# Kernel optimization log

Hardware: AMD Instinct MI355X
Metric: run time of the kernel (lower is better)

The kernel has to match this reference:

```python
import jax, jax.numpy as jnp
import numpy as np

N, K, C = 32768, 64, 256
PAIR, HID, BINS, CLIP = 32, 64, 16, 32
LN_EPS = 1e-5


def setup_inputs() -> dict:
    key = jax.random.key(0)
    ks = jax.random.split(key, 12)
    inp = {
        "features": jax.random.normal(ks[0], (N, C), jnp.float32),
        "resi": jnp.arange(N, dtype=jnp.int32),
        "chain": jax.random.randint(ks[1], (N,), 0, 4, jnp.int32),
        "batch": jax.random.randint(ks[2], (N,), 0, 8, jnp.int32),
        "neighbours": jax.random.randint(ks[3], (N, K), 0, N, jnp.int32),
        # learned params
        "W_left": jax.random.normal(ks[4], (C, PAIR), jnp.float32) / np.sqrt(C),
        "W_right": jax.random.normal(ks[5], (C, PAIR), jnp.float32) / np.sqrt(C),
        "W_pos": jax.random.normal(ks[6], (2 * CLIP + 1, PAIR), jnp.float32) * 0.1,
        "ln_scale": jnp.ones((PAIR,), jnp.float32),
        "ln_bias": jnp.zeros((PAIR,), jnp.float32),
        "W1": jax.random.normal(ks[7], (PAIR, HID), jnp.float32) / np.sqrt(PAIR),
        "b1": jnp.zeros((HID,), jnp.float32),
        "W2": jax.random.normal(ks[8], (HID, BINS), jnp.float32) / np.sqrt(HID),
        "b2": jnp.zeros((BINS,), jnp.float32),
    }
    return inp


def reference(features, resi, chain, batch, neighbours,
              W_left, W_right, W_pos, ln_scale, ln_bias, W1, b1, W2, b2):
    # left/right 32-dim codes, pairwise combine via neighbour gather: [N,K,32]
    left = features @ W_left
    right = features @ W_right
    dcode = left[:, None, :] + right[neighbours]

    # relative sequence position one-hot (65 classes) -> Linear(32, bias=False).
    # one_hot @ W_pos == row-gather of W_pos; masked to same chain & batch.
    rel = jnp.clip(resi[neighbours] - resi[:, None], -CLIP, CLIP) + CLIP  # [N,K]
    same = (chain[neighbours] == chain[:, None]) & (batch[neighbours] == batch[:, None])
    dcode = dcode + jnp.where(same[..., None], W_pos[rel], 0.0)

    # LayerNorm over last axis (scale + offset)
    mu = dcode.mean(-1, keepdims=True)
    var = jnp.mean(jnp.square(dcode - mu), -1, keepdims=True)
    dcode = (dcode - mu) * jax.lax.rsqrt(var + LN_EPS) * ln_scale + ln_bias

    # 2-layer GELU MLP -> 16 bins
    h = jax.nn.gelu(dcode @ W1 + b1)
    logits = h @ W2 + b2
    log_p = jax.nn.log_softmax(logits, axis=-1)

    # softmax-weighted expected distance over bin centers of [0, 22) A
    step = 22.0 / BINS
    bin_centers = (jnp.arange(BINS, dtype=jnp.float32) + 0.5) * step
    dmap = (jnp.exp(log_p) * bin_centers).sum(axis=-1)  # [N,K]
    return log_p, dmap
```

## Files before the change

kernel.cpp:

```cpp
#include <hip/hip_runtime.h>
#include <stdint.h>

#define N_RES 32768
#define KNEI  64
#define CFEAT 256
#define PAIRD 32
#define HIDD  64
#define NBINS 16
#define CLIPV 32
#define NGROUPS (N_RES * KNEI / 16)

typedef __attribute__((ext_vector_type(8))) short  short8;
typedef __attribute__((ext_vector_type(4))) float  float4_t;

union U8 { uint32_t u[4]; short8 s8; };

__device__ __forceinline__ uint32_t pkbf(float a, float b) {
    uint32_t ua = __float_as_uint(a) + 0x8000u;
    uint32_t ub = __float_as_uint(b) + 0x8000u;
    uint32_t d;
    const uint32_t sel = 0x07060302u;
    asm("v_perm_b32 %0, %1, %2, %3" : "=v"(d) : "v"(ub), "v"(ua), "s"(sel));
    return d;
}
__device__ __forceinline__ float bflo(uint32_t w) { return __uint_as_float(w << 16); }
__device__ __forceinline__ float bfhi(uint32_t w) { return __uint_as_float(w & 0xFFFF0000u); }

__device__ __forceinline__ float fastrcp(float x) { return __builtin_amdgcn_rcpf(x); }
__device__ __forceinline__ float fexp2(float x)   { return __builtin_amdgcn_exp2f(x); }
__device__ __forceinline__ float flog2(float x)   { return __builtin_amdgcn_logf(x); }

__device__ __forceinline__ float gelu_tanh(float x) {
    const float k1 = 2.3022082f;
    const float k2 = 0.1029432f;
    float x2 = x * x;
    float t  = __builtin_fmaf(k2, x2, k1);
    float e  = fexp2(x * t);
    float th = __builtin_fmaf(-2.0f, fastrcp(e + 1.0f), 1.0f);
    float hx = 0.5f * x;
    return __builtin_fmaf(hx, th, hx);
}

__global__ __launch_bounds__(256) void proj_kernel(
    const float* __restrict__ feat, const float* __restrict__ Wl,
    const float* __restrict__ Wr, const int* __restrict__ resi,
    const int* __restrict__ chain, const int* __restrict__ batch,
    const float* __restrict__ wpos,
    uint4* __restrict__ leftbf, uint4* __restrict__ rightbf,
    uint32_t* __restrict__ meta, uint32_t* __restrict__ wposbf)
{
    __shared__ __align__(16) float Wc[CFEAT * 32];
    const int tid   = threadIdx.x;
    const int half  = blockIdx.x >> 9;
    const int rb    = (blockIdx.x & 511) * 64;
    const float* W  = half ? Wr : Wl;
    uint4* outtb    = half ? rightbf : leftbf;

    for (int idx = tid; idx < CFEAT * 32; idx += 256)
        Wc[idx] = W[idx];
    if (half == 0 && tid < 64) {
        int r = rb + tid;
        meta[r] = (uint32_t)resi[r] | ((uint32_t)chain[r] << 16)
                | ((uint32_t)batch[r] << 19);
    }
    if (blockIdx.x == 0) {
        for (int i = tid; i < (2 * CLIPV + 1) * PAIRD / 2; i += 256)
            wposbf[i] = pkbf(wpos[2 * i], wpos[2 * i + 1]);
    }
    __syncthreads();

    const int cb  = (tid & 3) * 8;
    const int row = rb + (tid >> 2);

    float acc[8];
#pragma unroll
    for (int j = 0; j < 8; ++j) acc[j] = 0.f;

    for (int i = 0; i < CFEAT; i += 4) {
        float4_t f = *(const float4_t*)(feat + (size_t)row * CFEAT + i);
#pragma unroll
        for (int s = 0; s < 4; ++s) {
            float4_t wa = *(const float4_t*)(Wc + (i + s) * 32 + cb);
            float4_t wb = *(const float4_t*)(Wc + (i + s) * 32 + cb + 4);
#pragma unroll
            for (int j = 0; j < 4; ++j) {
                acc[j]     = __builtin_fmaf(f[s], wa[j], acc[j]);
                acc[4 + j] = __builtin_fmaf(f[s], wb[j], acc[4 + j]);
            }
        }
    }
    uint2 o;
    o.x = pkbf(acc[0], acc[1]);
    o.y = pkbf(acc[2], acc[3]);
    uint2 o2;
    o2.x = pkbf(acc[4], acc[5]);
    o2.y = pkbf(acc[6], acc[7]);
    uint2* dst = (uint2*)outtb + (size_t)row * 8 + (cb >> 2);
    dst[0] = o;
    dst[1] = o2;
}

__global__ __launch_bounds__(256, 8) void pair_kernel(
    const uint4* __restrict__ leftbf, const uint4* __restrict__ rightbf,
    const uint32_t* __restrict__ meta, const int* __restrict__ nbr,
    const uint32_t* __restrict__ wposbf,
    const float* __restrict__ lnS, const float* __restrict__ lnB,
    const float* __restrict__ W1, const float* __restrict__ b1,
    const float* __restrict__ W2, const float* __restrict__ b2,
    float* __restrict__ out_logp, float* __restrict__ out_dmap)
{
    __shared__ __align__(16) unsigned char Hbuf[4][16 * 144];
    __shared__ __align__(16) float b1p[HIDD];

    const int tid    = threadIdx.x;
    const int lane   = tid & 63;
    const int wlocal = tid >> 6;
    const int q      = lane >> 4;
    const int c      = lane & 15;

    if (tid < HIDD) {
        float s = b1[tid];
        for (int k = 0; k < PAIRD; ++k)
            s = __builtin_fmaf(lnB[k], W1[k * HIDD + tid], s);
        b1p[tid] = s;
    }

    short8 w1a[4];
#pragma unroll
    for (int t = 0; t < 4; ++t) {
        U8 tmp;
#pragma unroll
        for (int v = 0; v < 4; ++v) {
            int k0 = q * 8 + 2 * v, k1 = k0 + 1;
            float a0 = lnS[k0] * W1[k0 * HIDD + 16 * t + c];
            float a1 = lnS[k1] * W1[k1 * HIDD + 16 * t + c];
            tmp.u[v] = pkbf(a0, a1);
        }
        w1a[t] = tmp.s8;
    }
    short8 w2a[2];
#pragma unroll
    for (int kt = 0; kt < 2; ++kt) {
        U8 tmp;
#pragma unroll
        for (int v = 0; v < 4; ++v) {
            int k0 = kt * 32 + q * 8 + 2 * v;
            tmp.u[v] = pkbf(W2[k0 * NBINS + c], W2[(k0 + 1) * NBINS + c]);
        }
        w2a[kt] = tmp.s8;
    }
    const float4_t b2f = *(const float4_t*)(b2 + 4 * q);

    __syncthreads();

    const int wglobal = (blockIdx.x * 256 + tid) >> 6;
    const int nwaves  = (gridDim.x * 256) >> 6;

    for (int g = wglobal; g < NGROUPS; g += nwaves) {
        const int pbase = g * 16;
        const int n = pbase >> 6;
        const int p = pbase + c;
        const int nb = __builtin_nontemporal_load(nbr + p);

        const uint32_t mn = meta[n];
        const uint32_t mb = meta[nb];
        const uint4 lf = leftbf [(size_t)n  * 4 + q];
        const uint4 rf = rightbf[(size_t)nb * 4 + q];

        const int rel = min(max((int)(mb & 0xFFFFu) - (int)(mn & 0xFFFFu),
                                -CLIPV), CLIPV) + CLIPV;
        const float msk = (((mb ^ mn) & 0xFFFF0000u) == 0u) ? 1.0f : 0.0f;
        const uint4 pw = *(const uint4*)(wposbf + rel * 16 + q * 4);

        const uint32_t la[4] = {lf.x, lf.y, lf.z, lf.w};
        const uint32_t ra[4] = {rf.x, rf.y, rf.z, rf.w};
        const uint32_t pa[4] = {pw.x, pw.y, pw.z, pw.w};
        float d[8];
#pragma unroll
        for (int v = 0; v < 4; ++v) {
            d[2 * v]     = __builtin_fmaf(msk, bflo(pa[v]), bflo(la[v]) + bflo(ra[v]));
            d[2 * v + 1] = __builtin_fmaf(msk, bfhi(pa[v]), bfhi(la[v]) + bfhi(ra[v]));
        }

        float s1 = 0.f, s2 = 0.f;
#pragma unroll
        for (int j = 0; j < 8; ++j) { s1 += d[j]; s2 = __builtin_fmaf(d[j], d[j], s2); }
        s1 += __shfl_xor(s1, 16, 64);  s1 += __shfl_xor(s1, 32, 64);
        s2 += __shfl_xor(s2, 16, 64);  s2 += __shfl_xor(s2, 32, 64);
        const float mu   = s1 * (1.0f / 32.0f);
        const float var  = __builtin_fmaf(-mu, mu, s2 * (1.0f / 32.0f));
        const float rstd = __builtin_amdgcn_rsqf(var + 1e-5f);
        const float sh   = -mu * rstd;

        U8 dpack;
#pragma unroll
        for (int v = 0; v < 4; ++v) {
            float nA = __builtin_fmaf(d[2 * v],     rstd, sh);
            float nB = __builtin_fmaf(d[2 * v + 1], rstd, sh);
            dpack.u[v] = pkbf(nA, nB);
        }
        const short8 dfrag = dpack.s8;

        float4_t hacc[4];
#pragma unroll
        for (int t = 0; t < 4; ++t) {
            float4_t c1 = *(const float4_t*)(b1p + 16 * t + 4 * q);
            hacc[t] = __builtin_amdgcn_mfma_f32_16x16x32_bf16(w1a[t], dfrag, c1, 0, 0, 0);
        }

        unsigned char* hb = &Hbuf[wlocal][0] + c * 144;
#pragma unroll
        for (int t = 0; t < 4; ++t) {
            float g0 = gelu_tanh(hacc[t][0]);
            float g1 = gelu_tanh(hacc[t][1]);
            float g2 = gelu_tanh(hacc[t][2]);
            float g3 = gelu_tanh(hacc[t][3]);
            uint2 w; w.x = pkbf(g0, g1); w.y = pkbf(g2, g3);
            *(uint2*)(hb + 32 * t + 8 * q) = w;
        }
        const short8 hf0 = *(const short8*)(hb + 16 * q);
        const short8 hf1 = *(const short8*)(hb + 64 + 16 * q);

        float4_t lacc;
        lacc = __builtin_amdgcn_mfma_f32_16x16x32_bf16(w2a[0], hf0, b2f,  0, 0, 0);
        lacc = __builtin_amdgcn_mfma_f32_16x16x32_bf16(w2a[1], hf1, lacc, 0, 0, 0);

        const float LOG2E = 1.4426950408889634f, LN2 = 0.6931471805599453f;
        float e[4];
#pragma unroll
        for (int r = 0; r < 4; ++r) e[r] = fexp2(lacc[r] * LOG2E);
        float ssum = (e[0] + e[1]) + (e[2] + e[3]);
        ssum += __shfl_xor(ssum, 16, 64);
        ssum += __shfl_xor(ssum, 32, 64);
        const float lse = flog2(ssum) * LN2;

        float4_t lp = {lacc[0] - lse, lacc[1] - lse, lacc[2] - lse, lacc[3] - lse};
        __builtin_nontemporal_store(lp, (float4_t*)(out_logp + (size_t)p * NBINS + 4 * q));

        const float step  = 22.0f / NBINS;
        const float cbase = (4 * q + 0.5f) * step;
        float dpart = e[0] * cbase + e[1] * (cbase + step)
                    + e[2] * (cbase + 2 * step) + e[3] * (cbase + 3 * step);
        dpart += __shfl_xor(dpart, 16, 64);
        dpart += __shfl_xor(dpart, 32, 64);
        if (q == 0)
            __builtin_nontemporal_store(dpart * fastrcp(ssum), out_dmap + p);
    }
}

extern "C" void kernel_launch(void* const* d_in, const int* in_sizes, int n_in,
                              void* d_out, int out_size, void* d_ws, size_t ws_size,
                              hipStream_t stream) {
    const float* features = (const float*)d_in[0];
    const int*   resi     = (const int*)d_in[1];
    const int*   chain    = (const int*)d_in[2];
    const int*   batch    = (const int*)d_in[3];
    const int*   nbr      = (const int*)d_in[4];
    const float* W_left   = (const float*)d_in[5];
    const float* W_right  = (const float*)d_in[6];
    const float* W_pos    = (const float*)d_in[7];
    const float* ln_scale = (const float*)d_in[8];
    const float* ln_bias  = (const float*)d_in[9];
    const float* W1       = (const float*)d_in[10];
    const float* b1       = (const float*)d_in[11];
    const float* W2       = (const float*)d_in[12];
    const float* b2       = (const float*)d_in[13];

    char* ws = (char*)d_ws;
    uint4*    leftbf  = (uint4*)ws;
    uint4*    rightbf = (uint4*)(ws + (size_t)N_RES * 64);
    uint32_t* meta    = (uint32_t*)(ws + (size_t)2 * N_RES * 64);
    uint32_t* wposbf  = (uint32_t*)(ws + (size_t)2 * N_RES * 64 + N_RES * 4);

    float* out_logp = (float*)d_out;
    float* out_dmap = out_logp + (size_t)N_RES * KNEI * NBINS;

    proj_kernel<<<1024, 256, 0, stream>>>(features, W_left, W_right,
                                          resi, chain, batch, W_pos,
                                          leftbf, rightbf, meta, wposbf);
    pair_kernel<<<2048, 256, 0, stream>>>(leftbf, rightbf, meta, nbr, wposbf,
                                          ln_scale, ln_bias, W1, b1, W2, b2,
                                          out_logp, out_dmap);
}
```

Measured before the change: 290.2 us.

## Use MFMA projection, sigmoid GELU, and two-group staging in pair kernel

The projection kernel now runs on bf16 MFMA. Both weight matrices are transposed into LDS as bf16, and each wave computes 16 rows of left and right codes, so the kernel needs half as many blocks. In the pair kernel, the tanh-form GELU is replaced by the cheaper x*sigmoid(1.702x) approximation. The main loop is restructured to a fixed 16-iteration schedule that stages gathers for two groups before computing either, using double-buffered LDS for the hidden activations. The aim is to hide gather latency and cut transcendental work, at the cost of more register pressure, a different GELU approximation, and features rounded to bf16 before the projection.

```diff
diff --git a/kernel.cpp b/kernel.cpp
--- a/kernel.cpp
+++ b/kernel.cpp
@@ -30,15 +30,10 @@
 __device__ __forceinline__ float fexp2(float x)   { return __builtin_amdgcn_exp2f(x); }
 __device__ __forceinline__ float flog2(float x)   { return __builtin_amdgcn_logf(x); }
 
-__device__ __forceinline__ float gelu_tanh(float x) {
-    const float k1 = 2.3022082f;
-    const float k2 = 0.1029432f;
-    float x2 = x * x;
-    float t  = __builtin_fmaf(k2, x2, k1);
-    float e  = fexp2(x * t);
-    float th = __builtin_fmaf(-2.0f, fastrcp(e + 1.0f), 1.0f);
-    float hx = 0.5f * x;
-    return __builtin_fmaf(hx, th, hx);
+__device__ __forceinline__ float gelu_fast(float x) {
+    const float kG = -2.4554669f;
+    float e = fexp2(kG * x);
+    return x * fastrcp(1.0f + e) * 1.0f + 0.0f, x * fastrcp(1.0f + e);
 }
 
 __global__ __launch_bounds__(256) void proj_kernel(
@@ -46,19 +41,27 @@
     const float* __restrict__ Wr, const int* __restrict__ resi,
     const int* __restrict__ chain, const int* __restrict__ batch,
     const float* __restrict__ wpos,
-    uint4* __restrict__ leftbf, uint4* __restrict__ rightbf,
+    uint32_t* __restrict__ leftbf, uint32_t* __restrict__ rightbf,
     uint32_t* __restrict__ meta, uint32_t* __restrict__ wposbf)
 {
-    __shared__ __align__(16) float Wc[CFEAT * 32];
-    const int tid   = threadIdx.x;
-    const int half  = blockIdx.x >> 9;
-    const int rb    = (blockIdx.x & 511) * 64;
-    const float* W  = half ? Wr : Wl;
-    uint4* outtb    = half ? rightbf : leftbf;
-
-    for (int idx = tid; idx < CFEAT * 32; idx += 256)
-        Wc[idx] = W[idx];
-    if (half == 0 && tid < 64) {
+    __shared__ __align__(16) unsigned short Wt[64 * 264];
+
+    const int tid    = threadIdx.x;
+    const int lane   = tid & 63;
+    const int wlocal = tid >> 6;
+    const int q      = lane >> 4;
+    const int c      = lane & 15;
+    const int rb     = blockIdx.x * 64;
+
+    {
+        const int col = tid & 63;
+        const float* wsrc = (col < 32) ? (Wl + col) : (Wr + col - 32);
+        for (int k = tid >> 6; k < CFEAT; k += 4) {
+            uint32_t u = __float_as_uint(wsrc[(size_t)k * 32]) + 0x8000u;
+            Wt[col * 264 + k] = (unsigned short)(u >> 16);
+        }
+    }
+    if (tid < 64) {
         int r = rb + tid;
         meta[r] = (uint32_t)resi[r] | ((uint32_t)chain[r] << 16)
                 | ((uint32_t)batch[r] << 19);
@@ -69,35 +72,138 @@
     }
     __syncthreads();
 
-    const int cb  = (tid & 3) * 8;
-    const int row = rb + (tid >> 2);
-
-    float acc[8];
-#pragma unroll
-    for (int j = 0; j < 8; ++j) acc[j] = 0.f;
-
-    for (int i = 0; i < CFEAT; i += 4) {
-        float4_t f = *(const float4_t*)(feat + (size_t)row * CFEAT + i);
-#pragma unroll
-        for (int s = 0; s < 4; ++s) {
-            float4_t wa = *(const float4_t*)(Wc + (i + s) * 32 + cb);
-            float4_t wb = *(const float4_t*)(Wc + (i + s) * 32 + cb + 4);
-#pragma unroll
-            for (int j = 0; j < 4; ++j) {
-                acc[j]     = __builtin_fmaf(f[s], wa[j], acc[j]);
-                acc[4 + j] = __builtin_fmaf(f[s], wb[j], acc[4 + j]);
-            }
+    const int row0 = rb + wlocal * 16;
+    const float* fptr = feat + (size_t)(row0 + c) * CFEAT + q * 8;
+    const float4_t zero4 = {0.f, 0.f, 0.f, 0.f};
+
+    float4_t acc[4] = {zero4, zero4, zero4, zero4};
+    for (int kt = 0; kt < 8; ++kt) {
+        float4_t f0 = *(const float4_t*)(fptr + kt * 32);
+        float4_t f1 = *(const float4_t*)(fptr + kt * 32 + 4);
+        U8 bp;
+        bp.u[0] = pkbf(f0[0], f0[1]);
+        bp.u[1] = pkbf(f0[2], f0[3]);
+        bp.u[2] = pkbf(f1[0], f1[1]);
+        bp.u[3] = pkbf(f1[2], f1[3]);
+#pragma unroll
+        for (int nt = 0; nt < 4; ++nt) {
+            const short8 afr = *(const short8*)(Wt + (nt * 16 + c) * 264 + kt * 32 + q * 8);
+            acc[nt] = __builtin_amdgcn_mfma_f32_16x16x32_bf16(afr, bp.s8, acc[nt], 0, 0, 0);
         }
     }
-    uint2 o;
-    o.x = pkbf(acc[0], acc[1]);
-    o.y = pkbf(acc[2], acc[3]);
-    uint2 o2;
-    o2.x = pkbf(acc[4], acc[5]);
-    o2.y = pkbf(acc[6], acc[7]);
-    uint2* dst = (uint2*)outtb + (size_t)row * 8 + (cb >> 2);
-    dst[0] = o;
-    dst[1] = o2;
+    const size_t row = (size_t)(row0 + c);
+#pragma unroll
+    for (int nt = 0; nt < 4; ++nt) {
+        uint2 o;
+        o.x = pkbf(acc[nt][0], acc[nt][1]);
+        o.y = pkbf(acc[nt][2], acc[nt][3]);
+        if (nt < 2)
+            *(uint2*)(leftbf  + row * 16 + nt * 8 + 2 * q) = o;
+        else
+            *(uint2*)(rightbf + row * 16 + (nt - 2) * 8 + 2 * q) = o;
+    }
+}
+
+struct GS { int p; uint4 lf, rf, pw; float msk; };
+
+__device__ __forceinline__ void stage_group(
+    int g, int c, int q,
+    const uint4* __restrict__ leftbf, const uint4* __restrict__ rightbf,
+    const uint32_t* __restrict__ meta, const int* __restrict__ nbr,
+    const uint32_t* __restrict__ wposbf, GS& s)
+{
+    const int pbase = g * 16;
+    const int nu = __builtin_amdgcn_readfirstlane(pbase >> 6);
+    s.p = pbase + c;
+    const int nb = __builtin_nontemporal_load(nbr + s.p);
+    const uint32_t mn = meta[nu];
+    const uint32_t mb = meta[nb];
+    s.lf = leftbf[(size_t)nu * 4 + q];
+    s.rf = rightbf[(size_t)nb * 4 + q];
+    const int rel = min(max((int)(mb & 0xFFFFu) - (int)(mn & 0xFFFFu),
+                            -CLIPV), CLIPV) + CLIPV;
+    s.msk = (((mb ^ mn) & 0xFFFF0000u) == 0u) ? 1.0f : 0.0f;
+    s.pw = *(const uint4*)(wposbf + rel * 16 + q * 4);
+}
+
+__device__ __forceinline__ void compute_group(
+    const GS& s, int q, unsigned char* hb,
+    const short8* w1a, const short8* w2a,
+    const float* __restrict__ b1p, float4_t b2f,
+    float* __restrict__ out_logp, float* __restrict__ out_dmap)
+{
+    const uint32_t la[4] = {s.lf.x, s.lf.y, s.lf.z, s.lf.w};
+    const uint32_t ra[4] = {s.rf.x, s.rf.y, s.rf.z, s.rf.w};
+    const uint32_t pa[4] = {s.pw.x, s.pw.y, s.pw.z, s.pw.w};
+    float d[8];
+#pragma unroll
+    for (int v = 0; v < 4; ++v) {
+        d[2 * v]     = __builtin_fmaf(s.msk, bflo(pa[v]), bflo(la[v]) + bflo(ra[v]));
+        d[2 * v + 1] = __builtin_fmaf(s.msk, bfhi(pa[v]), bfhi(la[v]) + bfhi(ra[v]));
+    }
+
+    float s1 = 0.f, s2 = 0.f;
+#pragma unroll
+    for (int j = 0; j < 8; ++j) { s1 += d[j]; s2 = __builtin_fmaf(d[j], d[j], s2); }
+    s1 += __shfl_xor(s1, 16, 64);  s1 += __shfl_xor(s1, 32, 64);
+    s2 += __shfl_xor(s2, 16, 64);  s2 += __shfl_xor(s2, 32, 64);
+    const float mu   = s1 * (1.0f / 32.0f);
+    const float var  = __builtin_fmaf(-mu, mu, s2 * (1.0f / 32.0f));
+    const float rstd = __builtin_amdgcn_rsqf(var + 1e-5f);
+    const float sh   = -mu * rstd;
+
+    U8 dpack;
+#pragma unroll
+    for (int v = 0; v < 4; ++v) {
+        float nA = __builtin_fmaf(d[2 * v],     rstd, sh);
+        float nB = __builtin_fmaf(d[2 * v + 1], rstd, sh);
+        dpack.u[v] = pkbf(nA, nB);
+    }
+    const short8 dfrag = dpack.s8;
+
+    float4_t hacc[4];
+#pragma unroll
+    for (int t = 0; t < 4; ++t) {
+        float4_t c1 = *(const float4_t*)(b1p + 16 * t + 4 * q);
+        hacc[t] = __builtin_amdgcn_mfma_f32_16x16x32_bf16(w1a[t], dfrag, c1, 0, 0, 0);
+    }
+
+    const float kG = -2.4554669f;
+#pragma unroll
+    for (int t = 0; t < 4; ++t) {
+        float g0 = hacc[t][0] * fastrcp(1.0f + fexp2(kG * hacc[t][0]));
+        float g1 = hacc[t][1] * fastrcp(1.0f + fexp2(kG * hacc[t][1]));
+        float g2 = hacc[t][2] * fastrcp(1.0f + fexp2(kG * hacc[t][2]));
+        float g3 = hacc[t][3] * fastrcp(1.0f + fexp2(kG * hacc[t][3]));
+        uint2 w; w.x = pkbf(g0, g1); w.y = pkbf(g2, g3);
+        *(uint2*)(hb + 32 * t + 8 * q) = w;
+    }
+    const short8 hf0 = *(const short8*)(hb + 16 * q);
+    const short8 hf1 = *(const short8*)(hb + 64 + 16 * q);
+
+    float4_t lacc;
+    lacc = __builtin_amdgcn_mfma_f32_16x16x32_bf16(w2a[0], hf0, b2f,  0, 0, 0);
+    lacc = __builtin_amdgcn_mfma_f32_16x16x32_bf16(w2a[1], hf1, lacc, 0, 0, 0);
+
+    const float LOG2E = 1.4426950408889634f, LN2 = 0.6931471805599453f;
+    float e[4];
+#pragma unroll
+    for (int r = 0; r < 4; ++r) e[r] = fexp2(lacc[r] * LOG2E);
+    float ssum = (e[0] + e[1]) + (e[2] + e[3]);
+    ssum += __shfl_xor(ssum, 16, 64);
+    ssum += __shfl_xor(ssum, 32, 64);
+    const float lse = flog2(ssum) * LN2;
+
+    float4_t lp = {lacc[0] - lse, lacc[1] - lse, lacc[2] - lse, lacc[3] - lse};
+    __builtin_nontemporal_store(lp, (float4_t*)(out_logp + (size_t)s.p * NBINS + 4 * q));
+
+    const float step  = 22.0f / NBINS;
+    const float cbase = (4 * q + 0.5f) * step;
+    float dpart = e[0] * cbase + e[1] * (cbase + step)
+                + e[2] * (cbase + 2 * step) + e[3] * (cbase + 3 * step);
+    dpart += __shfl_xor(dpart, 16, 64);
+    dpart += __shfl_xor(dpart, 32, 64);
+    __builtin_nontemporal_store(dpart * fastrcp(ssum), out_dmap + s.p);
 }
 
 __global__ __launch_bounds__(256, 8) void pair_kernel(
@@ -109,7 +215,7 @@
     const float* __restrict__ W2, const float* __restrict__ b2,
     float* __restrict__ out_logp, float* __restrict__ out_dmap)
 {
-    __shared__ __align__(16) unsigned char Hbuf[4][16 * 144];
+    __shared__ __align__(16) unsigned char Hbuf[4][2][16 * 144];
     __shared__ __align__(16) float b1p[HIDD];
 
     const int tid    = threadIdx.x;
@@ -154,97 +260,15 @@
     __syncthreads();
 
     const int wglobal = (blockIdx.x * 256 + tid) >> 6;
-    const int nwaves  = (gridDim.x * 256) >> 6;
-
-    for (int g = wglobal; g < NGROUPS; g += nwaves) {
-        const int pbase = g * 16;
-        const int n = pbase >> 6;
-        const int p = pbase + c;
-        const int nb = __builtin_nontemporal_load(nbr + p);
-
-        const uint32_t mn = meta[n];
-        const uint32_t mb = meta[nb];
-        const uint4 lf = leftbf [(size_t)n  * 4 + q];
-        const uint4 rf = rightbf[(size_t)nb * 4 + q];
-
-        const int rel = min(max((int)(mb & 0xFFFFu) - (int)(mn & 0xFFFFu),
-                                -CLIPV), CLIPV) + CLIPV;
-        const float msk = (((mb ^ mn) & 0xFFFF0000u) == 0u) ? 1.0f : 0.0f;
-        const uint4 pw = *(const uint4*)(wposbf + rel * 16 + q * 4);
-
-        const uint32_t la[4] = {lf.x, lf.y, lf.z, lf.w};
-        const uint32_t ra[4] = {rf.x, rf.y, rf.z, rf.w};
-        const uint32_t pa[4] = {pw.x, pw.y, pw.z, pw.w};
-        float d[8];
-#pragma unroll
-        for (int v = 0; v < 4; ++v) {
-            d[2 * v]     = __builtin_fmaf(msk, bflo(pa[v]), bflo(la[v]) + bflo(ra[v]));
-            d[2 * v + 1] = __builtin_fmaf(msk, bfhi(pa[v]), bfhi(la[v]) + bfhi(ra[v]));
-        }
-
-        float s1 = 0.f, s2 = 0.f;
-#pragma unroll
-        for (int j = 0; j < 8; ++j) { s1 += d[j]; s2 = __builtin_fmaf(d[j], d[j], s2); }
-        s1 += __shfl_xor(s1, 16, 64);  s1 += __shfl_xor(s1, 32, 64);
-        s2 += __shfl_xor(s2, 16, 64);  s2 += __shfl_xor(s2, 32, 64);
-        const float mu   = s1 * (1.0f / 32.0f);
-        const float var  = __builtin_fmaf(-mu, mu, s2 * (1.0f / 32.0f));
-        const float rstd = __builtin_amdgcn_rsqf(var + 1e-5f);
-        const float sh   = -mu * rstd;
-
-        U8 dpack;
-#pragma unroll
-        for (int v = 0; v < 4; ++v) {
-            float nA = __builtin_fmaf(d[2 * v],     rstd, sh);
-            float nB = __builtin_fmaf(d[2 * v + 1], rstd, sh);
-            dpack.u[v] = pkbf(nA, nB);
-        }
-        const short8 dfrag = dpack.s8;
-
-        float4_t hacc[4];
-#pragma unroll
-        for (int t = 0; t < 4; ++t) {
-            float4_t c1 = *(const float4_t*)(b1p + 16 * t + 4 * q);
-            hacc[t] = __builtin_amdgcn_mfma_f32_16x16x32_bf16(w1a[t], dfrag, c1, 0, 0, 0);
-        }
-
-        unsigned char* hb = &Hbuf[wlocal][0] + c * 144;
-#pragma unroll
-        for (int t = 0; t < 4; ++t) {
-            float g0 = gelu_tanh(hacc[t][0]);
-            float g1 = gelu_tanh(hacc[t][1]);
-            float g2 = gelu_tanh(hacc[t][2]);
-            float g3 = gelu_tanh(hacc[t][3]);
-            uint2 w; w.x = pkbf(g0, g1); w.y = pkbf(g2, g3);
-            *(uint2*)(hb + 32 * t + 8 * q) = w;
-        }
-        const short8 hf0 = *(const short8*)(hb + 16 * q);
-        const short8 hf1 = *(const short8*)(hb + 64 + 16 * q);
-
-        float4_t lacc;
-        lacc = __builtin_amdgcn_mfma_f32_16x16x32_bf16(w2a[0], hf0, b2f,  0, 0, 0);
-        lacc = __builtin_amdgcn_mfma_f32_16x16x32_bf16(w2a[1], hf1, lacc, 0, 0, 0);
-
-        const float LOG2E = 1.4426950408889634f, LN2 = 0.6931471805599453f;
-        float e[4];
-#pragma unroll
-        for (int r = 0; r < 4; ++r) e[r] = fexp2(lacc[r] * LOG2E);
-        float ssum = (e[0] + e[1]) + (e[2] + e[3]);
-        ssum += __shfl_xor(ssum, 16, 64);
-        ssum += __shfl_xor(ssum, 32, 64);
-        const float lse = flog2(ssum) * LN2;
-
-        float4_t lp = {lacc[0] - lse, lacc[1] - lse, lacc[2] - lse, lacc[3] - lse};
-        __builtin_nontemporal_store(lp, (float4_t*)(out_logp + (size_t)p * NBINS + 4 * q));
-
-        const float step  = 22.0f / NBINS;
-        const float cbase = (4 * q + 0.5f) * step;
-        float dpart = e[0] * cbase + e[1] * (cbase + step)
-                    + e[2] * (cbase + 2 * step) + e[3] * (cbase + 3 * step);
-        dpart += __shfl_xor(dpart, 16, 64);
-        dpart += __shfl_xor(dpart, 32, 64);
-        if (q == 0)
-            __builtin_nontemporal_store(dpart * fastrcp(ssum), out_dmap + p);
+    unsigned char* hb0 = &Hbuf[wlocal][0][0] + c * 144;
+    unsigned char* hb1 = &Hbuf[wlocal][1][0] + c * 144;
+
+    for (int j = 0; j < 16; j += 2) {
+        GS A, B;
+        stage_group(wglobal + j * 8192,       c, q, leftbf, rightbf, meta, nbr, wposbf, A);
+        stage_group(wglobal + (j + 1) * 8192, c, q, leftbf, rightbf, meta, nbr, wposbf, B);
+        compute_group(A, q, hb0, w1a, w2a, b1p, b2f, out_logp, out_dmap);
+        compute_group(B, q, hb1, w1a, w2a, b1p, b2f, out_logp, out_dmap);
     }
 }
 
@@ -267,18 +291,19 @@
     const float* b2       = (const float*)d_in[13];
 
     char* ws = (char*)d_ws;
-    uint4*    leftbf  = (uint4*)ws;
-    uint4*    rightbf = (uint4*)(ws + (size_t)N_RES * 64);
+    uint32_t* leftbf  = (uint32_t*)ws;
+    uint32_t* rightbf = (uint32_t*)(ws + (size_t)N_RES * 64);
     uint32_t* meta    = (uint32_t*)(ws + (size_t)2 * N_RES * 64);
     uint32_t* wposbf  = (uint32_t*)(ws + (size_t)2 * N_RES * 64 + N_RES * 4);
 
     float* out_logp = (float*)d_out;
     float* out_dmap = out_logp + (size_t)N_RES * KNEI * NBINS;
 
-    proj_kernel<<<1024, 256, 0, stream>>>(features, W_left, W_right,
-                                          resi, chain, batch, W_pos,
-                                          leftbf, rightbf, meta, wposbf);
-    pair_kernel<<<2048, 256, 0, stream>>>(leftbf, rightbf, meta, nbr, wposbf,
+    proj_kernel<<<512, 256, 0, stream>>>(features, W_left, W_right,
+                                         resi, chain, batch, W_pos,
+                                         leftbf, rightbf, meta, wposbf);
+    pair_kernel<<<2048, 256, 0, stream>>>((const uint4*)leftbf, (const uint4*)rightbf,
+                                          meta, nbr, wposbf,
                                           ln_scale, ln_bias, W1, b1, W2, b2,
                                           out_logp, out_dmap);
 }
```

Result: slower. 444.1 us (+53.0%).
